# Kernel tuning notes

Hardware: AMD Instinct MI355X
Metric: run time of the kernel (lower is better)

Reference implementation:

```python
import jax, jax.numpy as jnp
import numpy as np

# SMPL kinematic tree (24 joints)
PARENTS = [-1, 0, 0, 0, 1, 2, 3, 4, 5, 6, 7, 8, 9, 9, 9, 12, 13, 14, 16, 17, 18, 19, 20, 21]
B, V, J, NB = 1024, 6890, 24, 10
POSE_BASIS = 9 * (J - 1)  # 207


def setup_inputs() -> dict:
    key = jax.random.key(0)
    ks = jax.random.split(key, 8)
    betas = jax.random.normal(ks[0], (B, NB), jnp.float32)
    global_rot = jax.random.normal(ks[1], (B, 1, 3, 3), jnp.float32)
    body_pose = jax.random.normal(ks[2], (B, J - 1, 3, 3), jnp.float32)
    v_template = jax.random.normal(ks[3], (V, 3), jnp.float32)
    shapedirs = jax.random.normal(ks[4], (V, 3, NB), jnp.float32) * 0.01
    posedirs = jax.random.normal(ks[5], (POSE_BASIS, V * 3), jnp.float32) * 0.01
    J_regressor = jax.random.uniform(ks[6], (J, V), jnp.float32) / V
    w = jax.random.uniform(ks[7], (V, J), jnp.float32)
    lbs_weights = w / w.sum(-1, keepdims=True)
    return dict(betas=betas, global_rot=global_rot, body_pose=body_pose,
                v_template=v_template, shapedirs=shapedirs, posedirs=posedirs,
                J_regressor=J_regressor, lbs_weights=lbs_weights)


def reference(betas, global_rot, body_pose, v_template, shapedirs, posedirs,
              J_regressor, lbs_weights):
    b = betas.shape[0]
    full_pose = jnp.concatenate([global_rot, body_pose], axis=1)  # [B,24,3,3]

    # shape blend shapes
    v_shaped = v_template + jnp.einsum('bl,vcl->bvc', betas, shapedirs)  # [B,V,3]
    Jt = jnp.einsum('jv,bvc->bjc', J_regressor, v_shaped)  # [B,24,3]

    # pose blend shapes (pose2rot=False: rotations given)
    eye3 = jnp.eye(3, dtype=betas.dtype)
    pose_feature = (full_pose[:, 1:] - eye3).reshape(b, POSE_BASIS)  # [B,207]
    v_posed = v_shaped + (pose_feature @ posedirs).reshape(b, V, 3)

    # forward kinematics along parent chain
    rel_joints = jnp.concatenate(
        [Jt[:, :1], Jt[:, 1:] - Jt[:, jnp.array(PARENTS[1:])]], axis=1)  # [B,24,3]
    top = jnp.concatenate([full_pose, rel_joints[..., None]], axis=-1)  # [B,24,3,4]
    bottom = jnp.broadcast_to(jnp.array([0., 0., 0., 1.], dtype=betas.dtype),
                              (b, J, 1, 4))
    T_local = jnp.concatenate([top, bottom], axis=-2)  # [B,24,4,4]

    chain = [T_local[:, 0]]
    for i in range(1, J):  # fixed small tree, sequential dependency
        chain.append(chain[PARENTS[i]] @ T_local[:, i])
    A = jnp.stack(chain, axis=1)  # [B,24,4,4]

    posed_joints = A[..., :3, 3]  # [B,24,3]
    # make transforms relative to rest-pose joints
    rel_t = posed_joints - jnp.einsum('bjmn,bjn->bjm', A[..., :3, :3], Jt)
    A_rel = A.at[..., :3, 3].set(rel_t)

    # linear blend skinning
    T = jnp.einsum('vj,bjmn->bvmn', lbs_weights, A_rel)  # [B,V,4,4]
    vertices = jnp.einsum('bvmn,bvn->bvm', T[..., :3, :3], v_posed) + T[..., :3, 3]
    return vertices, posed_joints
```

## Files before the change

kernel.cpp:

```cpp
#include <hip/hip_runtime.h>

#define BN 1024
#define NV 6890
#define NBETA 10
#define PB 207
#define N3 20670
#define NCOL 20736
#define NCHUNK 7
#define BT 32

typedef __bf16 bf16x8 __attribute__((ext_vector_type(8)));
typedef float  f32x4  __attribute__((ext_vector_type(4)));

__device__ __constant__ int c_par[24] = {-1,0,0,0,1,2,3,4,5,6,7,8,9,9,9,12,13,14,16,17,18,19,20,21};

__device__ inline unsigned short f2bf(float f) {
    unsigned u = __float_as_uint(f);
    u += 0x7fff + ((u >> 16) & 1);
    return (unsigned short)(u >> 16);
}

__device__ inline void dma16(const void* g, void* l) {
    __builtin_amdgcn_global_load_lds(
        (const __attribute__((address_space(1))) unsigned int*)g,
        (__attribute__((address_space(3))) unsigned int*)l, 16, 0, 0);
}

__global__ __launch_bounds__(256) void k_prep(const float* __restrict__ pd,
                                              const float* __restrict__ sd,
                                              const float* __restrict__ vtm,
                                              const float* __restrict__ Jr,
                                              const float* __restrict__ bpose,
                                              const float* __restrict__ betas,
                                              const float* __restrict__ w,
                                              unsigned short* __restrict__ ws_pdt,
                                              unsigned short* __restrict__ ws_pfb,
                                              unsigned short* __restrict__ ws_wb,
                                              float* __restrict__ ws_jsp)
{
    int blk = blockIdx.x;
    if (blk < 567) {
        int t = blk * 256 + threadIdx.x;
        int kc = t / NCOL;
        int col = t - kc * NCOL;
        bool cok = col < N3;
        unsigned short vals[40];
        #pragma unroll
        for (int kk = 0; kk < 32; kk++) {
            int gk = kc * 32 + kk;
            float val = 0.f;
            if (cok) {
                if (gk < PB)             val = pd[(size_t)gk * N3 + col];
                else if (gk < PB + 10)   val = sd[(size_t)col * NBETA + (gk - PB)];
                else if (gk == PB + 10)  val = vtm[col];
            }
            vals[kk] = f2bf(val);
        }
        #pragma unroll
        for (int kk = 32; kk < 40; kk++) vals[kk] = 0;
        uint4* dst = (uint4*)(ws_pdt + (size_t)t * 40);
        #pragma unroll
        for (int q = 0; q < 5; q++) {
            uint4 u;
            u.x = vals[q*8+0] | ((unsigned)vals[q*8+1] << 16);
            u.y = vals[q*8+2] | ((unsigned)vals[q*8+3] << 16);
            u.z = vals[q*8+4] | ((unsigned)vals[q*8+5] << 16);
            u.w = vals[q*8+6] | ((unsigned)vals[q*8+7] << 16);
            dst[q] = u;
        }
    } else if (blk < 799) {
        int e0 = (blk - 567) * 1024 + threadIdx.x * 4;
        unsigned short v4[4];
        #pragma unroll
        for (int r = 0; r < 4; r++) {
            int e = e0 + r;
            int b = e / 232, k = e - b * 232;
            float x = 0.f;
            if (k < PB) {
                x = bpose[(size_t)b * PB + k];
                int k9 = k % 9;
                if (k9 == 0 || k9 == 4 || k9 == 8) x -= 1.f;
            } else if (k < PB + 10) {
                x = betas[b * NBETA + (k - PB)];
            } else if (k == PB + 10) {
                x = 1.f;
            }
            v4[r] = f2bf(x);
        }
        uint2 u;
        u.x = v4[0] | ((unsigned)v4[1] << 16);
        u.y = v4[2] | ((unsigned)v4[3] << 16);
        *(uint2*)(ws_pfb + e0) = u;
    } else if (blk < 1069) {
        int e0 = (blk - 799) * 1024 + threadIdx.x * 4;
        unsigned short v4[4];
        #pragma unroll
        for (int r = 0; r < 4; r++) {
            int e = e0 + r;
            int v = e / 40, j = e - v * 40;
            float val = (j < 24 && v < NV) ? w[(size_t)v * 24 + j] : 0.f;
            v4[r] = f2bf(val);
        }
        uint2 u;
        u.x = v4[0] | ((unsigned)v4[1] << 16);
        u.y = v4[2] | ((unsigned)v4[3] << 16);
        *(uint2*)(ws_wb + e0) = u;
    } else {
        int b2 = blk - 1069;
        int jc = b2 >> 3;
        int seg = b2 & 7;
        int j = jc / 3, c = jc % 3;
        int v0 = seg * 862;
        int v1 = v0 + 862; if (v1 > NV) v1 = NV;

        float acc[11];
        #pragma unroll
        for (int l = 0; l < 11; l++) acc[l] = 0.f;

        for (int v = v0 + threadIdx.x; v < v1; v += 256) {
            float r = Jr[j * NV + v];
            acc[10] += r * vtm[v * 3 + c];
            const float* s = sd + (size_t)(v * 3 + c) * NBETA;
            #pragma unroll
            for (int l = 0; l < NBETA; l++) acc[l] += r * s[l];
        }

        __shared__ float red[4][11];
        int lane = threadIdx.x & 63, wv = threadIdx.x >> 6;
        #pragma unroll
        for (int l = 0; l < 11; l++) {
            float x = acc[l];
            x += __shfl_down(x, 32, 64);
            x += __shfl_down(x, 16, 64);
            x += __shfl_down(x, 8, 64);
            x += __shfl_down(x, 4, 64);
            x += __shfl_down(x, 2, 64);
            x += __shfl_down(x, 1, 64);
            if (lane == 0) red[wv][l] = x;
        }
        __syncthreads();
        if (threadIdx.x == 0) {
            #pragma unroll
            for (int l = 0; l < 11; l++)
                ws_jsp[((size_t)seg * 72 + jc) * 11 + l]
                    = red[0][l] + red[1][l] + red[2][l] + red[3][l];
        }
    }
}

__global__ __launch_bounds__(256) void k_chain(const float* __restrict__ betas,
                                               const float* __restrict__ grot,
                                               const float* __restrict__ bpose,
                                               const float* __restrict__ ws_jsp,
                                               unsigned short* __restrict__ ws_artb,
                                               float* __restrict__ pj)
{
    __shared__ float js_s[72 * 11];
    __shared__ float jt[16][72];
    __shared__ float tl[16][288];
    __shared__ float am[16][288];
    int tid = threadIdx.x;

    for (int e = tid; e < 72 * 11; e += 256) {
        float s = 0.f;
        #pragma unroll
        for (int seg = 0; seg < 8; seg++)
            s += ws_jsp[(size_t)seg * 792 + e];
        js_s[e] = s;
    }
    __syncthreads();

    int lb = tid >> 4;
    int e  = tid & 15;
    int b  = blockIdx.x * 16 + lb;

    for (int idx = e; idx < 72; idx += 16) {
        float acc = js_s[idx * 11 + 10];
        const float* be = betas + b * NBETA;
        #pragma unroll
        for (int l = 0; l < NBETA; l++) acc += be[l] * js_s[idx * 11 + l];
        jt[lb][idx] = acc;
    }
    __syncthreads();

    for (int idx = e; idx < 288; idx += 16) {
        int j = idx / 12, e12 = idx % 12, m = e12 >> 2, n = e12 & 3;
        float val;
        if (n < 3) {
            val = (j == 0) ? grot[(size_t)b * 9 + m * 3 + n]
                           : bpose[((size_t)b * 23 + (j - 1)) * 9 + m * 3 + n];
        } else {
            val = jt[lb][j * 3 + m];
            if (j > 0) val -= jt[lb][c_par[j] * 3 + m];
        }
        tl[lb][idx] = val;
    }
    __syncthreads();

    if (e < 12) am[lb][e] = tl[lb][e];
    for (int i = 1; i < 24; i++) {
        __syncthreads();
        if (e < 12) {
            int p = c_par[i];
            int m = e >> 2, n = e & 3;
            float val = am[lb][p*12 + m*4 + 0] * tl[lb][i*12 + 0 + n]
                      + am[lb][p*12 + m*4 + 1] * tl[lb][i*12 + 4 + n]
                      + am[lb][p*12 + m*4 + 2] * tl[lb][i*12 + 8 + n];
            if (n == 3) val += am[lb][p*12 + m*4 + 3];
            am[lb][i*12 + e] = val;
        }
    }
    __syncthreads();

    for (int idx = e; idx < 72; idx += 16) {
        int j = idx / 3, m = idx % 3;
        pj[(size_t)b * 72 + idx] = am[lb][j*12 + m*4 + 3];
    }
    for (int idx = e; idx < 480; idx += 16) {
        int col = idx / 40, j = idx - col * 40;
        float val = 0.f;
        if (j < 24) {
            int m = col >> 2, n = col & 3;
            if (n < 3) {
                val = am[lb][j*12 + col];
            } else {
                val = am[lb][j*12 + m*4 + 3]
                    - am[lb][j*12 + m*4 + 0] * jt[lb][j*3 + 0]
                    - am[lb][j*12 + m*4 + 1] * jt[lb][j*3 + 1]
                    - am[lb][j*12 + m*4 + 2] * jt[lb][j*3 + 2];
            }
        }
        ws_artb[(size_t)b * 480 + idx] = f2bf(val);
    }
}

__global__ __launch_bounds__(256, 3) void k_vert(const unsigned short* __restrict__ ws_pdt,
                                                 const unsigned short* __restrict__ ws_pfb,
                                                 const unsigned short* __restrict__ ws_wb,
                                                 const unsigned short* __restrict__ ws_artb,
                                                 float* __restrict__ out)
{
    const int bb = blockIdx.x;
    const int vb = blockIdx.y;
    const int tid = threadIdx.x;
    const int wv = tid >> 6;
    const int lane = tid & 63;
    const int r16 = lane & 15;
    const int half8 = (lane >> 4) * 8;

    __shared__ __align__(16) unsigned char smem[52992];
    unsigned short* pdT_l = (unsigned short*)smem;
    float*          disp_l = (float*)smem;
    unsigned short* ArT_l = (unsigned short*)(smem + 25088);
    float*          T_l   = (float*)(smem + 40448);

    {
        const unsigned short* srcA = ws_artb + (size_t)(bb * BT) * 480;
        for (int i = wv; i < 15; i += 4)
            dma16((const char*)srcA + i * 1024 + lane * 16, (char*)ArT_l + i * 1024);
        const unsigned short* srcP = ws_pdt + (size_t)vb * 192 * 40;
        for (int i = wv; i < 15; i += 4)
            dma16((const char*)srcP + i * 1024 + lane * 16, (char*)pdT_l + i * 1024);
    }

    const unsigned short* pfbase = ws_pfb + (size_t)(bb * BT) * 232;
    bf16x8 a0 = *(const bf16x8*)(pfbase + r16 * 232 + half8);
    bf16x8 a1 = *(const bf16x8*)(pfbase + (16 + r16) * 232 + half8);

    __syncthreads();

    f32x4 acc[2][3];
    #pragma unroll
    for (int mt = 0; mt < 2; mt++)
        #pragma unroll
        for (int t = 0; t < 3; t++)
            acc[mt][t] = (f32x4){0.f, 0.f, 0.f, 0.f};

    #pragma unroll
    for (int kc = 0; kc < NCHUNK; kc++) {
        bf16x8 b0 = *(const bf16x8*)(pdT_l + (wv * 48 + r16) * 40 + half8);
        bf16x8 b1 = *(const bf16x8*)(pdT_l + (wv * 48 + 16 + r16) * 40 + half8);
        bf16x8 b2 = *(const bf16x8*)(pdT_l + (wv * 48 + 32 + r16) * 40 + half8);
        bf16x8 a0n, a1n;
        if (kc < NCHUNK - 1) {
            a0n = *(const bf16x8*)(pfbase + r16 * 232 + (kc + 1) * 32 + half8);
            a1n = *(const bf16x8*)(pfbase + (16 + r16) * 232 + (kc + 1) * 32 + half8);
        }
        __syncthreads();
        if (kc < NCHUNK - 1) {
            const unsigned short* src = ws_pdt + ((size_t)(kc + 1) * NCOL + (size_t)vb * 192) * 40;
            for (int i = wv; i < 15; i += 4)
                dma16((const char*)src + i * 1024 + lane * 16, (char*)pdT_l + i * 1024);
        }
        acc[0][0] = __builtin_amdgcn_mfma_f32_16x16x32_bf16(a0, b0, acc[0][0], 0, 0, 0);
        acc[1][0] = __builtin_amdgcn_mfma_f32_16x16x32_bf16(a1, b0, acc[1][0], 0, 0, 0);
        acc[0][1] = __builtin_amdgcn_mfma_f32_16x16x32_bf16(a0, b1, acc[0][1], 0, 0, 0);
        acc[1][1] = __builtin_amdgcn_mfma_f32_16x16x32_bf16(a1, b1, acc[1][1], 0, 0, 0);
        acc[0][2] = __builtin_amdgcn_mfma_f32_16x16x32_bf16(a0, b2, acc[0][2], 0, 0, 0);
        acc[1][2] = __builtin_amdgcn_mfma_f32_16x16x32_bf16(a1, b2, acc[1][2], 0, 0, 0);
        a0 = a0n; a1 = a1n;
        if (kc < NCHUNK - 1) __syncthreads();
    }

    #pragma unroll
    for (int mt = 0; mt < 2; mt++) {
        #pragma unroll
        for (int t = 0; t < 3; t++) {
            int col = wv * 48 + t * 16 + r16;
            int brow = mt * 16 + (lane >> 4) * 4;
            #pragma unroll
            for (int r = 0; r < 4; r++)
                disp_l[(brow + r) * 196 + col] = acc[mt][t][r];
        }
    }
    __syncthreads();

    bf16x8 aw = *(const bf16x8*)(ws_wb + (size_t)(vb * 64 + wv * 16 + r16) * 40 + half8);

    const int vg = vb * 64 + lane;

    for (int half = 0; half < 2; half++) {
        if (half == 1) {
            const unsigned short* srcA = ws_artb + (size_t)(bb * BT + 16) * 480;
            for (int i = wv; i < 15; i += 4)
                dma16((const char*)srcA + i * 1024 + lane * 16, (char*)ArT_l + i * 1024);
            __syncthreads();
        }
        for (int s = 0; s < 4; s++) {
            int sub = half * 4 + s;
            bf16x8 bA0 = *(const bf16x8*)(ArT_l + (s * 48 + r16) * 40 + half8);
            bf16x8 bA1 = *(const bf16x8*)(ArT_l + (s * 48 + 16 + r16) * 40 + half8);
            bf16x8 bA2 = *(const bf16x8*)(ArT_l + (s * 48 + 32 + r16) * 40 + half8);
            f32x4 z = (f32x4){0.f, 0.f, 0.f, 0.f};
            f32x4 t0 = __builtin_amdgcn_mfma_f32_16x16x32_bf16(aw, bA0, z, 0, 0, 0);
            f32x4 t1 = __builtin_amdgcn_mfma_f32_16x16x32_bf16(aw, bA1, z, 0, 0, 0);
            f32x4 t2 = __builtin_amdgcn_mfma_f32_16x16x32_bf16(aw, bA2, z, 0, 0, 0);

            int vrow = wv * 16 + (lane >> 4) * 4;
            #pragma unroll
            for (int r = 0; r < 4; r++) {
                T_l[(vrow + r) * 49 + r16]      = t0[r];
                T_l[(vrow + r) * 49 + 16 + r16] = t1[r];
                T_l[(vrow + r) * 49 + 32 + r16] = t2[r];
            }
            __syncthreads();

            if (vg < NV) {
                const float* Tv = &T_l[lane * 49 + wv * 12];
                float x = disp_l[(sub * 4 + wv) * 196 + lane * 3 + 0];
                float y = disp_l[(sub * 4 + wv) * 196 + lane * 3 + 1];
                float zz = disp_l[(sub * 4 + wv) * 196 + lane * 3 + 2];
                size_t b = (size_t)(bb * BT + sub * 4 + wv);
                float* o = out + b * N3 + (size_t)vg * 3;
                o[0] = Tv[0] * x + Tv[1] * y + Tv[2]  * zz + Tv[3];
                o[1] = Tv[4] * x + Tv[5] * y + Tv[6]  * zz + Tv[7];
                o[2] = Tv[8] * x + Tv[9] * y + Tv[10] * zz + Tv[11];
            }
            __syncthreads();
        }
    }
}

extern "C" void kernel_launch(void* const* d_in, const int* in_sizes, int n_in,
                              void* d_out, int out_size, void* d_ws, size_t ws_size,
                              hipStream_t stream) {
    const float* betas = (const float*)d_in[0];
    const float* grot  = (const float*)d_in[1];
    const float* bpose = (const float*)d_in[2];
    const float* vtm   = (const float*)d_in[3];
    const float* sd    = (const float*)d_in[4];
    const float* pd    = (const float*)d_in[5];
    const float* Jr    = (const float*)d_in[6];
    const float* w     = (const float*)d_in[7];
    float* out = (float*)d_out;

    char* ws = (char*)d_ws;
    unsigned short* ws_pdt  = (unsigned short*)(ws);
    unsigned short* ws_pfb  = (unsigned short*)(ws + 11612160);
    unsigned short* ws_wb   = (unsigned short*)(ws + 12087296);
    float*          ws_jsp  = (float*)         (ws + 12640256);
    unsigned short* ws_artb = (unsigned short*)(ws + 12665600);

    k_prep<<<1645, 256, 0, stream>>>(pd, sd, vtm, Jr, bpose, betas, w,
                                     ws_pdt, ws_pfb, ws_wb, ws_jsp);
    k_chain<<<BN / 16, 256, 0, stream>>>(betas, grot, bpose, ws_jsp, ws_artb,
                                         out + (size_t)BN * N3);
    k_vert<<<dim3(32, 108), 256, 0, stream>>>(ws_pdt, ws_pfb, ws_wb, ws_artb, out);
}
```

Measured before the change: 187.8 us.

## Apply skinning transforms directly from MFMA registers via lane shuffles

The per-vertex skinning step no longer stages the MFMA transform results through an LDS buffer. Each lane multiplies its accumulator element by the matching displaced-vertex component, or by 1 for the translation column, and reduces across four lanes with xor shuffles. This drops the T_l staging area and two barriers per sub-step, and shrinks shared memory enough to raise the launch bound to four blocks per CU. In exchange, only a quarter of lanes write, each storing a scattered single float, so global stores are less coalesced.

```diff
diff --git a/kernel.cpp b/kernel.cpp
--- a/kernel.cpp
+++ b/kernel.cpp
@@ -234,7 +234,7 @@
     }
 }
 
-__global__ __launch_bounds__(256, 3) void k_vert(const unsigned short* __restrict__ ws_pdt,
+__global__ __launch_bounds__(256, 4) void k_vert(const unsigned short* __restrict__ ws_pdt,
                                                  const unsigned short* __restrict__ ws_pfb,
                                                  const unsigned short* __restrict__ ws_wb,
                                                  const unsigned short* __restrict__ ws_artb,
@@ -248,11 +248,10 @@
     const int r16 = lane & 15;
     const int half8 = (lane >> 4) * 8;
 
-    __shared__ __align__(16) unsigned char smem[52992];
+    __shared__ __align__(16) unsigned char smem[40448];
     unsigned short* pdT_l = (unsigned short*)smem;
     float*          disp_l = (float*)smem;
     unsigned short* ArT_l = (unsigned short*)(smem + 25088);
-    float*          T_l   = (float*)(smem + 40448);
 
     {
         const unsigned short* srcA = ws_artb + (size_t)(bb * BT) * 480;
@@ -317,10 +316,19 @@
 
     bf16x8 aw = *(const bf16x8*)(ws_wb + (size_t)(vb * 64 + wv * 16 + r16) * 40 + half8);
 
-    const int vg = vb * 64 + lane;
+    const int vbase = wv * 16 + (half8 >> 1);
+    const int n = r16 & 3;
+    int bl[3], mm[3];
+    #pragma unroll
+    for (int t = 0; t < 3; t++) {
+        int q = 4 * t + (r16 >> 2);
+        bl[t] = (q * 11) >> 5;
+        mm[t] = q - 3 * bl[t];
+    }
 
     for (int half = 0; half < 2; half++) {
         if (half == 1) {
+            __syncthreads();
             const unsigned short* srcA = ws_artb + (size_t)(bb * BT + 16) * 480;
             for (int i = wv; i < 15; i += 4)
                 dma16((const char*)srcA + i * 1024 + lane * 16, (char*)ArT_l + i * 1024);
@@ -336,27 +344,23 @@
             f32x4 t1 = __builtin_amdgcn_mfma_f32_16x16x32_bf16(aw, bA1, z, 0, 0, 0);
             f32x4 t2 = __builtin_amdgcn_mfma_f32_16x16x32_bf16(aw, bA2, z, 0, 0, 0);
 
-            int vrow = wv * 16 + (lane >> 4) * 4;
             #pragma unroll
-            for (int r = 0; r < 4; r++) {
-                T_l[(vrow + r) * 49 + r16]      = t0[r];
-                T_l[(vrow + r) * 49 + 16 + r16] = t1[r];
-                T_l[(vrow + r) * 49 + 32 + r16] = t2[r];
+            for (int t = 0; t < 3; t++) {
+                f32x4 tt = (t == 0) ? t0 : (t == 1) ? t1 : t2;
+                const float* drow = disp_l + (sub * 4 + bl[t]) * 196 + vbase * 3 + n;
+                size_t obase = (size_t)(bb * BT + sub * 4 + bl[t]) * N3
+                             + (size_t)(vb * 64 + vbase) * 3 + mm[t];
+                int vg0 = vb * 64 + vbase;
+                #pragma unroll
+                for (int r = 0; r < 4; r++) {
+                    float vh = (n < 3) ? drow[r * 3] : 1.0f;
+                    float p = tt[r] * vh;
+                    p += __shfl_xor(p, 1);
+                    p += __shfl_xor(p, 2);
+                    if (n == 0 && (vg0 + r) < NV)
+                        out[obase + (size_t)r * 3] = p;
+                }
             }
-            __syncthreads();
-
-            if (vg < NV) {
-                const float* Tv = &T_l[lane * 49 + wv * 12];
-                float x = disp_l[(sub * 4 + wv) * 196 + lane * 3 + 0];
-                float y = disp_l[(sub * 4 + wv) * 196 + lane * 3 + 1];
-                float zz = disp_l[(sub * 4 + wv) * 196 + lane * 3 + 2];
-                size_t b = (size_t)(bb * BT + sub * 4 + wv);
-                float* o = out + b * N3 + (size_t)vg * 3;
-                o[0] = Tv[0] * x + Tv[1] * y + Tv[2]  * zz + Tv[3];
-                o[1] = Tv[4] * x + Tv[5] * y + Tv[6]  * zz + Tv[7];
-                o[2] = Tv[8] * x + Tv[9] * y + Tv[10] * zz + Tv[11];
-            }
-            __syncthreads();
         }
     }
 }
```

Result: slower. 210.9 us (+12.3%).
